# Kernel optimization log

Measured on AMD Instinct MI355X. Metric: run time of the kernel, lower is better.

## Reference

```python
import jax, jax.numpy as jnp
import numpy as np

D_MODEL = 1024
D_STATE = 16
D_CONV = 4
EXPAND = 2
D_INNER = EXPAND * D_MODEL          # 2048
DT_RANK = D_MODEL // 16             # 64 (math.ceil(d_model/16))
BATCH, SEQLEN = 2, 1024


def setup_inputs() -> dict:
    key = jax.random.key(0)
    ks = jax.random.split(key, 9)
    f32 = jnp.float32
    hidden_states = jax.random.normal(ks[0], (BATCH, SEQLEN, D_MODEL), dtype=f32)
    in_proj_w = jax.random.normal(ks[1], (2 * D_INNER, D_MODEL), dtype=f32) * (D_MODEL ** -0.5)
    conv1d_w = jax.random.normal(ks[2], (D_INNER, D_CONV), dtype=f32) * (D_CONV ** -0.5)
    conv1d_b = jax.random.normal(ks[3], (D_INNER,), dtype=f32) * 0.1
    x_proj_w = jax.random.normal(ks[4], (DT_RANK + 2 * D_STATE, D_INNER), dtype=f32) * (D_INNER ** -0.5)
    dt_std = DT_RANK ** -0.5
    dt_proj_w = jax.random.uniform(ks[5], (D_INNER, DT_RANK), dtype=f32, minval=-dt_std, maxval=dt_std)
    dt_proj_b = jax.random.normal(ks[6], (D_INNER,), dtype=f32) * 0.1
    # A = repeat(arange(1, d_state+1), 'n -> d n'); A_log = log(A)
    A_log = jnp.log(jnp.tile(jnp.arange(1, D_STATE + 1, dtype=f32), (D_INNER, 1)))
    D_param = jnp.ones((D_INNER,), dtype=f32)
    out_proj_w = jax.random.normal(ks[7], (D_MODEL, D_INNER), dtype=f32) * (D_INNER ** -0.5)
    return dict(hidden_states=hidden_states, in_proj_w=in_proj_w, conv1d_w=conv1d_w,
                conv1d_b=conv1d_b, x_proj_w=x_proj_w, dt_proj_w=dt_proj_w,
                dt_proj_b=dt_proj_b, A_log=A_log, D_param=D_param, out_proj_w=out_proj_w)


def _mamba_fwd(hidden_states, in_proj_w, conv1d_w, conv1d_b, x_proj_w,
               dt_proj_w, dt_proj_b, A_log, D_param, out_proj_w):
    Bsz, L, _ = hidden_states.shape
    # in_proj: (B,L,d_model) -> (B,L,2*d_inner); split into x, z
    xz = jnp.einsum('bld,ed->ble', hidden_states, in_proj_w)
    x, z = jnp.split(xz, 2, axis=-1)                      # each (B,L,d_inner)
    # causal depthwise conv1d over L (left pad d_conv-1), then SiLU (fused in causal_conv1d_fwd)
    xc = jnp.transpose(x, (0, 2, 1))                      # (B,d_inner,L)
    kern = conv1d_w[:, None, :]                           # (d_inner,1,d_conv)
    conv = jax.lax.conv_general_dilated(
        xc, kern, window_strides=(1,), padding=[(D_CONV - 1, 0)],
        dimension_numbers=('NCH', 'OIH', 'NCH'), feature_group_count=D_INNER)
    u = jax.nn.silu(conv + conv1d_b[None, :, None])       # (B,d_inner,L)
    ut = jnp.transpose(u, (0, 2, 1))                      # (B,L,d_inner)
    # x_proj -> [dt | B | C]
    x_dbl = jnp.einsum('bld,rd->blr', ut, x_proj_w)       # (B,L,dt_rank+2*d_state)
    dt_low = x_dbl[..., :DT_RANK]
    B_var = x_dbl[..., DT_RANK:DT_RANK + D_STATE]         # (B,L,d_state)
    C_var = x_dbl[..., DT_RANK + D_STATE:]                # (B,L,d_state)
    # delta = softplus(dt_proj_w @ dt_low + dt_proj_b)  (delta_bias applied inside selective scan)
    delta = jax.nn.softplus(jnp.einsum('blr,dr->bld', dt_low, dt_proj_w) + dt_proj_b)  # (B,L,d_inner)
    A = -jnp.exp(A_log)                                   # (d_inner,d_state)
    # discretize: h_l = exp(delta*A) * h_{l-1} + (delta*B_l) * u_l
    dA = jnp.exp(delta[..., None] * A)                    # (B,L,d_inner,d_state)
    dBu = delta[..., None] * B_var[:, :, None, :] * ut[..., None]  # (B,L,d_inner,d_state)

    def step(h, inp):
        da, dbu, c = inp
        h = da * h + dbu                                  # (B,d_inner,d_state)
        y = jnp.einsum('bdn,bn->bd', h, c)
        return h, y

    h0 = jnp.zeros((Bsz, D_INNER, D_STATE), dtype=hidden_states.dtype)
    _, ys = jax.lax.scan(step, h0, (jnp.moveaxis(dA, 1, 0),
                                    jnp.moveaxis(dBu, 1, 0),
                                    jnp.moveaxis(C_var, 1, 0)))
    y = jnp.moveaxis(ys, 0, 1)                            # (B,L,d_inner)
    y = y + ut * D_param                                  # skip term D*u
    out_z = y * jax.nn.silu(z)                            # gated output
    return jnp.einsum('bld,ed->ble', out_z, out_proj_w)   # (B,L,d_model)


def reference(hidden_states, in_proj_w, conv1d_w, conv1d_b, x_proj_w,
              dt_proj_w, dt_proj_b, A_log, D_param, out_proj_w):
    return _mamba_fwd(hidden_states, in_proj_w, conv1d_w, conv1d_b, x_proj_w,
                      dt_proj_w, dt_proj_b, A_log, D_param, out_proj_w)
```

## Files before the change

kernel.cpp:

```cpp
#include <hip/hip_runtime.h>
#include <hip/hip_bf16.h>

#define BATCH 2
#define SEQLEN 1024
#define DMODEL 1024
#define DINNER 2048
#define DSTATE 16
#define DTRANK 64
#define ROWS (BATCH * SEQLEN)
#define LOG2E 1.44269504088896340736f

using bf16 = __hip_bfloat16;
typedef __bf16 bf16x8 __attribute__((ext_vector_type(8)));
typedef float f32x4 __attribute__((ext_vector_type(4)));
typedef unsigned short us8 __attribute__((ext_vector_type(8)));

__device__ __forceinline__ float to_f(float x) { return x; }
__device__ __forceinline__ float to_f(bf16 x) { return __bfloat162float(x); }

__device__ __forceinline__ float fexp2(float x) { return __builtin_amdgcn_exp2f(x); }

__device__ __forceinline__ float bfu(unsigned short u) {
    union { unsigned int i; float f; } v;
    v.i = ((unsigned int)u) << 16;
    return v.f;
}

__device__ __forceinline__ unsigned short bf_bits(float x) {
    bf16 h = __float2bfloat16(x);
    union { bf16 b; unsigned short u; } cv;
    cv.b = h;
    return cv.u;
}

__device__ __forceinline__ float softplus_f(float x) {
    return fmaxf(x, 0.f) + log1pf(expf(-fabsf(x)));
}
__device__ __forceinline__ float silu_f(float x) {
    return x * __builtin_amdgcn_rcpf(1.f + fexp2(-x * LOG2E));
}

template <int CTRL>
__device__ __forceinline__ float dpp_shr(float x) {
    int r = __builtin_amdgcn_update_dpp(0, __builtin_bit_cast(int, x), CTRL, 0xF, 0xF, false);
    return __builtin_bit_cast(float, r);
}
__device__ __forceinline__ float row16_sum_to_lane15(float p) {
    p += dpp_shr<0x111>(p);
    p += dpp_shr<0x112>(p);
    p += dpp_shr<0x114>(p);
    p += dpp_shr<0x118>(p);
    return p;
}

__device__ __forceinline__ void gload16(const void* g, void* l) {
    __builtin_amdgcn_global_load_lds(
        (const __attribute__((address_space(1))) void*)g,
        (__attribute__((address_space(3))) void*)l, 16, 0, 0);
}

__global__ __launch_bounds__(256) void prep_kernel(const unsigned short* hs, int* flag,
                                                   float* zbuf, int nzero) {
    if (blockIdx.x == 0) {
        __shared__ int cnt[256];
        int c = 0;
        for (int i = threadIdx.x; i < 8192; i += 256) {
            int e = (hs[i] >> 7) & 0xFF;
            if (e == 0 || e == 0xFF || e < 96 || e > 159) c++;
        }
        cnt[threadIdx.x] = c;
        __syncthreads();
        for (int s = 128; s > 0; s >>= 1) {
            if (threadIdx.x < s) cnt[threadIdx.x] += cnt[threadIdx.x + s];
            __syncthreads();
        }
        if (threadIdx.x == 0) *flag = (cnt[0] < 512) ? 1 : 0;
    } else {
        int i = (blockIdx.x - 1) * 256 + threadIdx.x;
        if (i < nzero) zbuf[i] = 0.f;
    }
}

struct SrcPtrs { const void* p[10]; };

__device__ __constant__ const size_t SEG_OFF[11] = {
    0, 2097152, 6291456, 6299648, 6301696, 6498304,
    6629376, 6631424, 6664192, 6666240, 8763392
};

__global__ __launch_bounds__(256) void convert_all(SrcPtrs s, bf16* __restrict__ dst,
                                                   const int* __restrict__ flag) {
    size_t e = ((size_t)blockIdx.x * 256 + threadIdx.x) * 4;
    if (e >= SEG_OFF[10]) return;
    int seg = 0;
    #pragma unroll
    for (int i = 1; i < 10; ++i) if (e >= SEG_OFF[i]) seg = i;
    int isbf = *flag;
    if (isbf && (seg == 0 || seg == 1 || seg == 9)) return;
    size_t loc = e - SEG_OFF[seg];
    if (isbf) {
        ushort4 v = ((const ushort4*)s.p[seg])[loc / 4];
        ((ushort4*)(dst + e))[0] = v;
    } else {
        float4 v = ((const float4*)s.p[seg])[loc / 4];
        ushort4 o;
        o.x = bf_bits(v.x); o.y = bf_bits(v.y);
        o.z = bf_bits(v.z); o.w = bf_bits(v.w);
        ((ushort4*)(dst + e))[0] = o;
    }
}

template <int OUTMODE>
__global__ __launch_bounds__(256) void gemm_mfma(
    const bf16* __restrict__ A, int lda,
    const bf16* __restrict__ Bm, int ldb,
    void* __restrict__ C, int ldc,
    int Kspl, size_t pstride,
    const bf16* __restrict__ bias,
    const bf16* __restrict__ Aalt,
    const bf16* __restrict__ Balt,
    const int* __restrict__ flag)
{
    if (flag && *flag) {
        if (Aalt) A = Aalt;
        if (Balt) Bm = Balt;
    }
    __shared__ __align__(16) __bf16 sA[128 * 32];
    __shared__ __align__(16) __bf16 sB[128 * 32];
    const int tid = threadIdx.x;
    const int m0 = blockIdx.y * 128;
    const int n0 = blockIdx.x * 128;
    const int wid = tid >> 6, ln = tid & 63;
    const int wy = (wid >> 1) * 64, wx = (wid & 1) * 64;
    const int q = ln >> 4, m16 = ln & 15;
    const int kbeg = blockIdx.z * Kspl;

    f32x4 acc[4][4] = {};

    for (int k0 = kbeg; k0 < kbeg + Kspl; k0 += 32) {
        #pragma unroll
        for (int i = 0; i < 2; ++i) {
            int idx = tid + i * 256;
            int r = idx >> 2, c = (idx & 3) * 8;
            gload16(&A[(size_t)(m0 + r) * lda + k0 + c], &sA[idx * 8]);
        }
        #pragma unroll
        for (int i = 0; i < 2; ++i) {
            int idx = tid + i * 256;
            int r = idx >> 2, c = (idx & 3) * 8;
            gload16(&Bm[(size_t)(n0 + r) * ldb + k0 + c], &sB[idx * 8]);
        }
        __syncthreads();
        bf16x8 a[4], b[4];
        #pragma unroll
        for (int i = 0; i < 4; ++i)
            a[i] = *(const bf16x8*)&sA[(wy + i * 16 + m16) * 32 + q * 8];
        #pragma unroll
        for (int j = 0; j < 4; ++j)
            b[j] = *(const bf16x8*)&sB[(wx + j * 16 + m16) * 32 + q * 8];
        #pragma unroll
        for (int i = 0; i < 4; ++i)
            #pragma unroll
            for (int j = 0; j < 4; ++j)
                acc[i][j] = __builtin_amdgcn_mfma_f32_16x16x32_bf16(a[i], b[j], acc[i][j], 0, 0, 0);
        __syncthreads();
    }

    #pragma unroll
    for (int i = 0; i < 4; ++i) {
        #pragma unroll
        for (int j = 0; j < 4; ++j) {
            #pragma unroll
            for (int r = 0; r < 4; ++r) {
                int row = m0 + wy + i * 16 + q * 4 + r;
                int col = n0 + wx + j * 16 + m16;
                size_t idx = (size_t)row * ldc + col;
                float v = acc[i][j][r];
                if constexpr (OUTMODE == 0) {
                    ((bf16*)C)[idx] = __float2bfloat16(v);
                } else if constexpr (OUTMODE == 2) {
                    ((float*)C + blockIdx.z * pstride)[idx] = v;
                } else if constexpr (OUTMODE == 3) {
                    if (col < 96) atomicAdd((float*)C + idx, v);
                } else if constexpr (OUTMODE == 4) {
                    ((float*)C)[idx] = softplus_f(v + to_f(bias[row]));
                }
            }
        }
    }
}

__global__ __launch_bounds__(256) void sum_store(
    const float* __restrict__ p0, const float* __restrict__ p1,
    void* __restrict__ out, const int* __restrict__ flag, int n4)
{
    int i = blockIdx.x * 256 + threadIdx.x;
    if (i >= n4) return;
    float4 a = ((const float4*)p0)[i];
    float4 b = ((const float4*)p1)[i];
    float4 sv; sv.x = a.x + b.x; sv.y = a.y + b.y; sv.z = a.z + b.z; sv.w = a.w + b.w;
    if (*flag) {
        ushort4 o;
        o.x = bf_bits(sv.x); o.y = bf_bits(sv.y);
        o.z = bf_bits(sv.z); o.w = bf_bits(sv.w);
        ((ushort4*)out)[i] = o;
    } else {
        ((float4*)out)[i] = sv;
    }
}

__global__ __launch_bounds__(256) void transpose_bf16(
    const ushort* __restrict__ src,
    ushort* __restrict__ dst)
{
    __shared__ ushort t[64][65];
    const int bx = blockIdx.x;
    const int by = blockIdx.y;
    const int tid = threadIdx.x;
    const int lr = tid & 63;
    const int ld = tid >> 6;
    #pragma unroll
    for (int i = 0; i < 16; ++i) {
        int d = ld + i * 4;
        t[d][lr] = src[(size_t)(by * 64 + d) * ROWS + bx * 64 + lr];
    }
    __syncthreads();
    #pragma unroll
    for (int i = 0; i < 16; ++i) {
        int r = ld + i * 4;
        dst[(size_t)(bx * 64 + r) * DINNER + by * 64 + lr] = t[lr][r];
    }
}

__global__ __launch_bounds__(256) void xd_cvt(
    const float* __restrict__ xd,
    bf16* __restrict__ xd_bf)
{
    int i = blockIdx.x * 256 + threadIdx.x;
    float4 v = ((const float4*)xd)[i];
    ushort4 o;
    o.x = bf_bits(v.x); o.y = bf_bits(v.y);
    o.z = bf_bits(v.z); o.w = bf_bits(v.w);
    ((ushort4*)xd_bf)[i] = o;
}

__global__ __launch_bounds__(256) void conv_silu_T8(
    const bf16* __restrict__ xzT,
    const bf16* __restrict__ w,
    const bf16* __restrict__ bias,
    bf16* __restrict__ utT)
{
    int t = blockIdx.x * 256 + threadIdx.x;
    int r0 = (t * 8) & (ROWS - 1);
    int d = t >> 8;

    const ushort* xp = (const ushort*)xzT + (size_t)d * ROWS + r0;
    float x[11];
    us8 cur = *(const us8*)xp;
    #pragma unroll
    for (int j = 0; j < 8; ++j) x[3 + j] = bfu(cur[j]);
    if ((r0 & (SEQLEN - 1)) != 0) {
        ushort4 pv = *(const ushort4*)(xp - 4);
        x[0] = bfu(pv.y); x[1] = bfu(pv.z); x[2] = bfu(pv.w);
    } else {
        x[0] = x[1] = x[2] = 0.f;
    }

    ushort4 wv = *(const ushort4*)((const ushort*)w + d * 4);
    float w0 = bfu(wv.x), w1 = bfu(wv.y), w2 = bfu(wv.z), w3 = bfu(wv.w);
    float bv = to_f(bias[d]);

    us8 o;
    #pragma unroll
    for (int j = 0; j < 8; ++j) {
        float acc = bv;
        acc = fmaf(x[j],     w0, acc);
        acc = fmaf(x[j + 1], w1, acc);
        acc = fmaf(x[j + 2], w2, acc);
        acc = fmaf(x[j + 3], w3, acc);
        o[j] = bf_bits(silu_f(acc));
    }
    *(us8*)((ushort*)utT + (size_t)d * ROWS + r0) = o;
}

#define SCHUNK 16
#define SSTEPS (SEQLEN / SCHUNK)
__global__ __launch_bounds__(1024) void scan_kernel15(
    const float* __restrict__ deltaT,
    const bf16*  __restrict__ utT,
    const float* __restrict__ xd96,
    const bf16*  __restrict__ xzT,
    const bf16*  __restrict__ A_log,
    const bf16*  __restrict__ Dp,
    bf16* __restrict__ outzT)
{
    __shared__ float2 sHP[SCHUNK][64];
    __shared__ float sQ[SCHUNK][4][68];
    __shared__ float sS[SCHUNK][4][68];
    const int tid = threadIdx.x;
    const int c = tid >> 6;
    const int w = tid & 63;
    const int dcol = (tid >> 4) & 3;
    const int n = tid & 15;
    const int b = blockIdx.x >> 9;
    const int d = ((blockIdx.x & 511) << 2) + dcol;
    const int row0 = b * SEQLEN + c * SSTEPS;

    const float Aa2 = -expf(to_f(A_log[d * DSTATE + n])) * LOG2E;
    const float Dv = to_f(Dp[d]);

    const float*  dp = deltaT + (size_t)d * ROWS + row0;
    const ushort* up = (const ushort*)utT + (size_t)d * ROWS + row0;
    const ushort* zp = (const ushort*)xzT + (size_t)(DINNER + d) * ROWS + row0;
    const float*  bcp = xd96 + (size_t)row0 * 96 + 64 + n;

    float hl = 0.f, sd = 0.f;
    float4  dv4 = *(const float4*)(dp);
    ushort4 uv4 = *(const ushort4*)(up);
    const float* bct = bcp;
    for (int i0 = 0; i0 < SSTEPS; i0 += 4) {
        float4  dvn = *(const float4*)(dp + i0 + 4);
        ushort4 uvn = *(const ushort4*)(up + i0 + 4);
        float Bv[4], Cv[4];
        Bv[0] = bct[0];   Cv[0] = bct[16];
        Bv[1] = bct[96];  Cv[1] = bct[112];
        Bv[2] = bct[192]; Cv[2] = bct[208];
        Bv[3] = bct[288]; Cv[3] = bct[304];
        bct += 384;
        float dv[4] = {dv4.x, dv4.y, dv4.z, dv4.w};
        float uv[4] = {bfu(uv4.x), bfu(uv4.y), bfu(uv4.z), bfu(uv4.w)};
        float qv[4], sv[4];
        #pragma unroll
        for (int j = 0; j < 4; ++j) {
            sd += dv[j];
            sv[j] = sd;
            float a = fexp2(dv[j] * Aa2);
            hl = fmaf(a, hl, dv[j] * Bv[j] * uv[j]);
            float p = hl * Cv[j];
            p = row16_sum_to_lane15(p);
            qv[j] = fmaf(uv[j], Dv, p);
        }
        if (n == 15) {
            float4 qo; qo.x = qv[0]; qo.y = qv[1]; qo.z = qv[2]; qo.w = qv[3];
            float4 so; so.x = sv[0]; so.y = sv[1]; so.z = sv[2]; so.w = sv[3];
            *(float4*)&sQ[c][dcol][i0] = qo;
            *(float4*)&sS[c][dcol][i0] = so;
        }
        dv4 = dvn; uv4 = uvn;
    }
    sHP[c][w] = make_float2(hl, fexp2(sd * Aa2));
    __syncthreads();

    float hin = 0.f;
    for (int cc = 0; cc < c; ++cc) {
        float2 hp = sHP[cc][w];
        hin = fmaf(hp.y, hin, hp.x);
    }

    ushort4 zv4 = *(const ushort4*)(zp);
    bct = bcp;
    for (int i0 = 0; i0 < SSTEPS; i0 += 4) {
        ushort4 zvn = *(const ushort4*)(zp + i0 + 4);
        float Cv[4];
        Cv[0] = bct[16];  Cv[1] = bct[112];
        Cv[2] = bct[208]; Cv[3] = bct[304];
        bct += 384;
        float4 q4 = *(const float4*)&sQ[c][dcol][i0];
        float4 s4 = *(const float4*)&sS[c][dcol][i0];
        float ss[4] = {s4.x, s4.y, s4.z, s4.w};
        float qq[4] = {q4.x, q4.y, q4.z, q4.w};
        float zv[4] = {bfu(zv4.x), bfu(zv4.y), bfu(zv4.z), bfu(zv4.w)};
        float y[4];
        #pragma unroll
        for (int j = 0; j < 4; ++j) {
            float e = fexp2(ss[j] * Aa2);
            float p = (hin * e) * Cv[j];
            p = row16_sum_to_lane15(p);
            y[j] = qq[j] + p;
        }
        if (n == 15) {
            ushort4 o;
            o.x = bf_bits(y[0] * silu_f(zv[0]));
            o.y = bf_bits(y[1] * silu_f(zv[1]));
            o.z = bf_bits(y[2] * silu_f(zv[2]));
            o.w = bf_bits(y[3] * silu_f(zv[3]));
            *(ushort4*)((ushort*)outzT + (size_t)d * ROWS + row0 + i0) = o;
        }
        zv4 = zvn;
    }
}

extern "C" void kernel_launch(void* const* d_in, const int* in_sizes, int n_in,
                              void* d_out, int out_size, void* d_ws, size_t ws_size,
                              hipStream_t stream) {
    static const size_t SZ[10] = {
        (size_t)BATCH * SEQLEN * DMODEL,
        (size_t)2 * DINNER * DMODEL,
        (size_t)DINNER * 4,
        (size_t)DINNER,
        (size_t)(DTRANK + 2 * DSTATE) * DINNER,
        (size_t)DINNER * DTRANK,
        (size_t)DINNER,
        (size_t)DINNER * DSTATE,
        (size_t)DINNER,
        (size_t)DMODEL * DINNER
    };
    size_t tot_in = 0;
    for (int i = 0; i < 10; ++i) tot_in += SZ[i];

    char* p = (char*)d_ws;
    int* flag = (int*)p;                     p += 64;
    bf16* inb = (bf16*)p;                    p += tot_in * 2;
    bf16* xzT = (bf16*)p;                    p += (size_t)4096 * ROWS * 2;
    bf16* utT = (bf16*)p;                    p += (size_t)DINNER * ROWS * 2;
    bf16* ut  = (bf16*)p;                    p += (size_t)ROWS * DINNER * 2;
    float* xd = (float*)p;                   p += (size_t)ROWS * 96 * 4;
    bf16* xd_bf = (bf16*)p;                  p += (size_t)ROWS * 96 * 2;
    float* deltaT = (float*)p;               p += (size_t)DINNER * ROWS * 4;
    bf16* outzT = (bf16*)p;                  p += (size_t)DINNER * ROWS * 2;
    bf16* outz = (bf16*)p;                   p += (size_t)ROWS * DINNER * 2;
    float* part = (float*)p;                 p += (size_t)2 * ROWS * DMODEL * 4;
    size_t needed = (size_t)(p - (char*)d_ws);
    if (ws_size < needed) return;

    dim3 blk(256);

    prep_kernel<<<1 + (ROWS * 96 + 255) / 256, blk, 0, stream>>>(
        (const unsigned short*)d_in[0], flag, xd, ROWS * 96);

    bf16* inp[10];
    {
        size_t off = 0;
        for (int i = 0; i < 10; ++i) { inp[i] = inb + off; off += SZ[i]; }
    }
    SrcPtrs sp;
    for (int i = 0; i < 10; ++i) sp.p[i] = d_in[i];
    convert_all<<<(int)((tot_in / 4 + 255) / 256), blk, 0, stream>>>(sp, inb, flag);

    const bf16* hs        = inp[0];
    const bf16* in_proj_w = inp[1];
    const bf16* conv_w    = inp[2];
    const bf16* conv_b    = inp[3];
    const bf16* x_proj_w  = inp[4];
    const bf16* dt_proj_w = inp[5];
    const bf16* dt_proj_b = inp[6];
    const bf16* A_log     = inp[7];
    const bf16* Dp        = inp[8];
    const bf16* out_proj_w= inp[9];

    gemm_mfma<0><<<dim3(ROWS / 128, 4096 / 128, 1), blk, 0, stream>>>(
        in_proj_w, DMODEL, hs, DMODEL, xzT, ROWS, DMODEL, 0, nullptr,
        (const bf16*)d_in[1], (const bf16*)d_in[0], flag);

    conv_silu_T8<<<(DINNER * ROWS / 8) / 256, blk, 0, stream>>>(xzT, conv_w, conv_b, utT);

    transpose_bf16<<<dim3(ROWS / 64, DINNER / 64), blk, 0, stream>>>(
        (const ushort*)utT, (ushort*)ut);

    gemm_mfma<3><<<dim3(1, ROWS / 128, 4), blk, 0, stream>>>(
        ut, DINNER, x_proj_w, DINNER, xd, 96, DINNER / 4, 0, nullptr,
        nullptr, nullptr, nullptr);

    xd_cvt<<<ROWS * 96 / 4 / 256, blk, 0, stream>>>(xd, xd_bf);

    gemm_mfma<4><<<dim3(ROWS / 128, DINNER / 128, 1), blk, 0, stream>>>(
        dt_proj_w, DTRANK, xd_bf, 96, deltaT, ROWS, DTRANK, 0, dt_proj_b,
        nullptr, nullptr, nullptr);

    scan_kernel15<<<BATCH * (DINNER / 4), dim3(1024), 0, stream>>>(
        deltaT, utT, xd, xzT, A_log, Dp, outzT);

    transpose_bf16<<<dim3(ROWS / 64, DINNER / 64), blk, 0, stream>>>(
        (const ushort*)outzT, (ushort*)outz);

    gemm_mfma<2><<<dim3(DMODEL / 128, ROWS / 128, 2), blk, 0, stream>>>(
        outz, DINNER, out_proj_w, DINNER, part, DMODEL, DINNER / 2, (size_t)ROWS * DMODEL,
        nullptr, nullptr, (const bf16*)d_in[9], flag);

    sum_store<<<(ROWS * DMODEL / 4 + 255) / 256, blk, 0, stream>>>(
        part, part + (size_t)ROWS * DMODEL, d_out, flag, ROWS * DMODEL / 4);
}
```

Before: 300.9 us.

## Restructure chunked scan to recompute states in second pass

The chunked selective scan now uses a lighter first pass that only computes each chunk's end state and decay product, with no output reduction or shared-memory staging. After the cross-chunk carry is combined, a second pass reruns the recurrence from the carried-in state and produces outputs directly, dropping the sQ/sS shared buffers and the exp of prefix sums. Chunk count drops from 16 to 8, so blocks shrink to 512 threads and each thread walks twice as many timesteps. The trade is more serial work per thread, and delta, u and B are read twice, in exchange for fewer cross-lane reductions and less shared memory.

```diff
diff --git a/kernel.cpp b/kernel.cpp
--- a/kernel.cpp
+++ b/kernel.cpp
@@ -283,9 +283,9 @@
     *(us8*)((ushort*)utT + (size_t)d * ROWS + r0) = o;
 }
 
-#define SCHUNK 16
+#define SCHUNK 8
 #define SSTEPS (SEQLEN / SCHUNK)
-__global__ __launch_bounds__(1024) void scan_kernel15(
+__global__ __launch_bounds__(512) void scan_kernel16(
     const float* __restrict__ deltaT,
     const bf16*  __restrict__ utT,
     const float* __restrict__ xd96,
@@ -295,8 +295,6 @@
     bf16* __restrict__ outzT)
 {
     __shared__ float2 sHP[SCHUNK][64];
-    __shared__ float sQ[SCHUNK][4][68];
-    __shared__ float sS[SCHUNK][4][68];
     const int tid = threadIdx.x;
     const int c = tid >> 6;
     const int w = tid & 63;
@@ -321,6 +319,40 @@
     for (int i0 = 0; i0 < SSTEPS; i0 += 4) {
         float4  dvn = *(const float4*)(dp + i0 + 4);
         ushort4 uvn = *(const ushort4*)(up + i0 + 4);
+        float Bv[4];
+        Bv[0] = bct[0];
+        Bv[1] = bct[96];
+        Bv[2] = bct[192];
+        Bv[3] = bct[288];
+        bct += 384;
+        float dv[4] = {dv4.x, dv4.y, dv4.z, dv4.w};
+        float uv[4] = {bfu(uv4.x), bfu(uv4.y), bfu(uv4.z), bfu(uv4.w)};
+        #pragma unroll
+        for (int j = 0; j < 4; ++j) {
+            sd += dv[j];
+            float a = fexp2(dv[j] * Aa2);
+            hl = fmaf(a, hl, dv[j] * Bv[j] * uv[j]);
+        }
+        dv4 = dvn; uv4 = uvn;
+    }
+    sHP[c][w] = make_float2(hl, fexp2(sd * Aa2));
+    __syncthreads();
+
+    float hin = 0.f;
+    for (int cc = 0; cc < c; ++cc) {
+        float2 hp = sHP[cc][w];
+        hin = fmaf(hp.y, hin, hp.x);
+    }
+
+    float h = hin;
+    dv4 = *(const float4*)(dp);
+    uv4 = *(const ushort4*)(up);
+    ushort4 zv4 = *(const ushort4*)(zp);
+    bct = bcp;
+    for (int i0 = 0; i0 < SSTEPS; i0 += 4) {
+        float4  dvn = *(const float4*)(dp + i0 + 4);
+        ushort4 uvn = *(const ushort4*)(up + i0 + 4);
+        ushort4 zvn = *(const ushort4*)(zp + i0 + 4);
         float Bv[4], Cv[4];
         Bv[0] = bct[0];   Cv[0] = bct[16];
         Bv[1] = bct[96];  Cv[1] = bct[112];
@@ -329,54 +361,15 @@
         bct += 384;
         float dv[4] = {dv4.x, dv4.y, dv4.z, dv4.w};
         float uv[4] = {bfu(uv4.x), bfu(uv4.y), bfu(uv4.z), bfu(uv4.w)};
-        float qv[4], sv[4];
-        #pragma unroll
-        for (int j = 0; j < 4; ++j) {
-            sd += dv[j];
-            sv[j] = sd;
-            float a = fexp2(dv[j] * Aa2);
-            hl = fmaf(a, hl, dv[j] * Bv[j] * uv[j]);
-            float p = hl * Cv[j];
-            p = row16_sum_to_lane15(p);
-            qv[j] = fmaf(uv[j], Dv, p);
-        }
-        if (n == 15) {
-            float4 qo; qo.x = qv[0]; qo.y = qv[1]; qo.z = qv[2]; qo.w = qv[3];
-            float4 so; so.x = sv[0]; so.y = sv[1]; so.z = sv[2]; so.w = sv[3];
-            *(float4*)&sQ[c][dcol][i0] = qo;
-            *(float4*)&sS[c][dcol][i0] = so;
-        }
-        dv4 = dvn; uv4 = uvn;
-    }
-    sHP[c][w] = make_float2(hl, fexp2(sd * Aa2));
-    __syncthreads();
-
-    float hin = 0.f;
-    for (int cc = 0; cc < c; ++cc) {
-        float2 hp = sHP[cc][w];
-        hin = fmaf(hp.y, hin, hp.x);
-    }
-
-    ushort4 zv4 = *(const ushort4*)(zp);
-    bct = bcp;
-    for (int i0 = 0; i0 < SSTEPS; i0 += 4) {
-        ushort4 zvn = *(const ushort4*)(zp + i0 + 4);
-        float Cv[4];
-        Cv[0] = bct[16];  Cv[1] = bct[112];
-        Cv[2] = bct[208]; Cv[3] = bct[304];
-        bct += 384;
-        float4 q4 = *(const float4*)&sQ[c][dcol][i0];
-        float4 s4 = *(const float4*)&sS[c][dcol][i0];
-        float ss[4] = {s4.x, s4.y, s4.z, s4.w};
-        float qq[4] = {q4.x, q4.y, q4.z, q4.w};
         float zv[4] = {bfu(zv4.x), bfu(zv4.y), bfu(zv4.z), bfu(zv4.w)};
         float y[4];
         #pragma unroll
         for (int j = 0; j < 4; ++j) {
-            float e = fexp2(ss[j] * Aa2);
-            float p = (hin * e) * Cv[j];
+            float a = fexp2(dv[j] * Aa2);
+            h = fmaf(a, h, dv[j] * Bv[j] * uv[j]);
+            float p = h * Cv[j];
             p = row16_sum_to_lane15(p);
-            y[j] = qq[j] + p;
+            y[j] = fmaf(uv[j], Dv, p);
         }
         if (n == 15) {
             ushort4 o;
@@ -386,7 +379,7 @@
             o.w = bf_bits(y[3] * silu_f(zv[3]));
             *(ushort4*)((ushort*)outzT + (size_t)d * ROWS + row0 + i0) = o;
         }
-        zv4 = zvn;
+        dv4 = dvn; uv4 = uvn; zv4 = zvn;
     }
 }
 
@@ -467,7 +460,7 @@
         dt_proj_w, DTRANK, xd_bf, 96, deltaT, ROWS, DTRANK, 0, dt_proj_b,
         nullptr, nullptr, nullptr);
 
-    scan_kernel15<<<BATCH * (DINNER / 4), dim3(1024), 0, stream>>>(
+    scan_kernel16<<<BATCH * (DINNER / 4), dim3(512), 0, stream>>>(
         deltaT, utT, xd, xzT, A_log, Dp, outzT);
 
     transpose_bf16<<<dim3(ROWS / 64, DINNER / 64), blk, 0, stream>>>(
```

Measured after the change: 294.2 us. -2.2%, faster.
